# Optimization experiments

Hardware: AMD Instinct MI355X
Metric: run time of the kernel (lower is better)

The kernel has to match this reference:

```python
import jax, jax.numpy as jnp
import numpy as np

R = 45        # num_dep_rels
L = 384       # sent_len
D = 512       # word representation dim = in_size*2
E_REL = 15    # dep_rel_emb_size
IN4 = 1024    # in_size*4
HOPS = 3
THRESH = 1e-06


def setup_inputs() -> dict:
    key = jax.random.key(0)
    ks = jax.random.split(key, 10)
    energy = jax.random.uniform(ks[0], (1, R, L, L), dtype=jnp.float32)
    word_h = jax.random.normal(ks[1], (1, L, D), dtype=jnp.float32)
    e1 = jax.random.normal(ks[2], (D,), dtype=jnp.float32)
    e2 = jax.random.normal(ks[3], (D,), dtype=jnp.float32)
    # learned params
    rel_embs = jax.random.normal(ks[4], (R, E_REL), dtype=jnp.float32)
    Wc = jax.random.normal(ks[5], (2 * D + E_REL, D), dtype=jnp.float32) * 0.02
    bc = jnp.zeros((D,), dtype=jnp.float32)
    Wk = jax.random.normal(ks[6], (HOPS, IN4, IN4), dtype=jnp.float32) * 0.02
    bk = jnp.zeros((HOPS, IN4), dtype=jnp.float32)
    Wh = jax.random.normal(ks[7], (HOPS, IN4, IN4), dtype=jnp.float32) * 0.02
    bh = jnp.zeros((HOPS, IN4), dtype=jnp.float32)
    return {"energy": energy, "word_h": word_h, "e1": e1, "e2": e2,
            "sent_len": L, "rel_embs": rel_embs, "Wc": Wc, "bc": bc,
            "Wk": Wk, "bk": bk, "Wh": Wh, "bh": bh}


def reference(energy, word_h, e1, e2, sent_len, rel_embs, Wc, bc, Wk, bk, Wh, bh):
    Ls = sent_len
    E = energy[0, :, :Ls, :Ls]                 # [R, L, L]
    marg = E.sum(axis=0)                       # [L, L] marginal energy
    # threshold back-off (try t, t/10, t/100 until some arc survives)
    m0 = marg > THRESH
    m1 = marg > THRESH * 0.1
    m2 = marg > THRESH * 0.01
    mask = jnp.where(m0.any(), m0, jnp.where(m1.any(), m1, m2))  # [L, L]

    H = word_h[0, :Ls]                         # [L, D]
    w = marg.reshape(-1)                       # [L*L] arc weights
    # rel embedding per arc: sum_r E[r,h,d] * rel_embs[r,e]
    rels = jnp.einsum('rhd,re->hde', E, rel_embs).reshape(Ls * Ls, E_REL)
    head_t = jnp.repeat(H, Ls, axis=0) * w[:, None]   # [L*L, D]
    dep_t = jnp.tile(H, (Ls, 1)) * w[:, None]         # [L*L, D]
    arc_in = jnp.concatenate([head_t, rels, dep_t], axis=1)  # [L*L, 2D+15]
    mem_bank = jax.nn.leaky_relu(arc_in @ Wc + bc)    # [L*L, D] (dropout=eval)
    maskf = mask.reshape(-1)                          # [L*L]

    # multi-hop memory attention; filtered-out arcs get zero attention weight
    inputs = jnp.concatenate([e1, e2])                # [1024]
    for i in range(HOPS):
        kv = inputs @ Wk[i] + bk[i]                   # [1024]
        k_, v_ = jnp.split(kv, 2)                     # chunk along dim 0
        k_ = jnp.tanh(k_)
        v_ = jax.nn.leaky_relu(v_)
        scores = jnp.where(maskf, mem_bank @ k_, -1e30)  # [L*L]
        dist = jax.nn.softmax(scores)
        mem_rep = dist @ mem_bank                     # [D]
        inputs = jax.nn.leaky_relu(jnp.concatenate([v_, mem_rep]) @ Wh[i] + bh[i])
    return inputs
```

## Files before the change

### kernel.cpp

```cpp
#include <hip/hip_runtime.h>
#include <hip/hip_bf16.h>
#include <cstdint>
#include <cstddef>

#define LL      147456
#define NBLK    768
#define CHB     12
#define NPACK   288

typedef __attribute__((ext_vector_type(8))) short  short8;
typedef __attribute__((ext_vector_type(4))) float  f32x4;

#define EPACK_OFF   0u
#define MARG_OFF    14155776u
#define A_OFF       14745600u
#define BTC_OFF     15532032u
#define UTGP_OFF    16318464u
#define XIN_OFF     16367616u
#define KBUF_OFF    16371712u
#define VBUF_OFF    16373760u
#define PM_OFF      16377856u
#define PL_OFF      16380928u
#define PACC_OFF    16384000u
#define BLKF_OFF    17956864u

#define SKIP_LD     20.0f
#define PV_EPS      1e-8f

static __device__ __forceinline__ ushort f2bf(float x) {
  uint u = __float_as_uint(x);
  return (ushort)((u + 0x7fffu + ((u >> 16) & 1u)) >> 16);
}
static __device__ __forceinline__ float lrelu(float x) { return fmaxf(x, 0.01f * x); }

__global__ __launch_bounds__(256) void k_prep(
    const float* __restrict__ E, uint4* __restrict__ ep,
    float* __restrict__ marg, int* __restrict__ blkflags,
    const float* __restrict__ H, const float* __restrict__ Wc,
    const float* __restrict__ rel, const float* __restrict__ bc,
    float* __restrict__ A, float* __restrict__ Btc, uint4* __restrict__ Utgp) {
  __shared__ float Hs[4][512];
  __shared__ float Ps[4][512];
  __shared__ int fsh;
  int b = blockIdx.x, t = threadIdx.x;
  if (b < 192) {
    bool roleA = (b < 96);
    int g0 = (roleA ? b : b - 96) * 4;
    const float* Wcp = Wc + (size_t)(roleA ? 0 : 527) * 512;
    for (int i = t; i < 4 * 512; i += 256) Hs[i >> 9][i & 511] = H[(size_t)g0 * 512 + i];
    __syncthreads();
    int cq = t & 127, q = t >> 7;
    int c0 = cq * 4;
    f32x4 acc[4];
#pragma unroll
    for (int i = 0; i < 4; ++i) acc[i] = (f32x4){0.f, 0.f, 0.f, 0.f};
    for (int k = q * 256; k < q * 256 + 256; ++k) {
      f32x4 wv = *(const f32x4*)&Wcp[(size_t)k * 512 + c0];
#pragma unroll
      for (int i = 0; i < 4; ++i) { float hv = Hs[i][k]; acc[i] += hv * wv; }
    }
    if (q == 1) {
#pragma unroll
      for (int i = 0; i < 4; ++i) *(f32x4*)&Ps[i][c0] = acc[i];
    }
    __syncthreads();
    if (q == 0) {
#pragma unroll
      for (int i = 0; i < 4; ++i) {
        acc[i] += *(const f32x4*)&Ps[i][c0];
        if (roleA) {
          *(f32x4*)&A[(size_t)(g0 + i) * 512 + c0] = acc[i];
        } else {
#pragma unroll
          for (int j = 0; j < 4; ++j) Btc[(size_t)(c0 + j) * 384 + (g0 + i)] = acc[i][j];
        }
      }
    }
  } else if (b == 192) {
    for (int c = t; c < 512; c += 256) {
      float uv[48];
#pragma unroll
      for (int k = 0; k < 45; ++k) {
        float s = 0.f;
#pragma unroll
        for (int e = 0; e < 15; ++e) s += rel[k * 15 + e] * Wc[(size_t)(512 + e) * 512 + c];
        uv[k] = s;
      }
      uv[45] = bc[c]; uv[46] = 0.f; uv[47] = 0.f;
#pragma unroll
      for (int g = 0; g < 6; ++g) {
        uint w[4];
#pragma unroll
        for (int p = 0; p < 4; ++p)
          w[p] = (uint)f2bf(uv[g * 8 + 2 * p]) | ((uint)f2bf(uv[g * 8 + 2 * p + 1]) << 16);
        uint4 v; v.x = w[0]; v.y = w[1]; v.z = w[2]; v.w = w[3];
        Utgp[g * 512 + c] = v;
      }
    }
  } else {
    if (t == 0) fsh = 0;
    int bp = b - 193;
    size_t hd0 = (size_t)bp * 512 + 2 * t;
    float2 ev[46];
#pragma unroll
    for (int r = 0; r < 45; ++r) ev[r] = *(const float2*)&E[(size_t)r * LL + hd0];
    ev[45] = make_float2(1.0f, 1.0f);
    float s0 = 0.f, s1 = 0.f;
#pragma unroll
    for (int r = 0; r < 45; ++r) { s0 += ev[r].x; s1 += ev[r].y; }
#pragma unroll
    for (int o = 0; o < 6; ++o) {
      uint wa[4], wb[4];
#pragma unroll
      for (int p = 0; p < 4; ++p) {
        int r0 = 8 * o + 2 * p, r1 = r0 + 1;
        float a0 = (r0 < 46) ? ev[r0].x : 0.f, a1 = (r1 < 46) ? ev[r1].x : 0.f;
        float b0 = (r0 < 46) ? ev[r0].y : 0.f, b1 = (r1 < 46) ? ev[r1].y : 0.f;
        wa[p] = (uint)f2bf(a0) | ((uint)f2bf(a1) << 16);
        wb[p] = (uint)f2bf(b0) | ((uint)f2bf(b1) << 16);
      }
      uint4 va; va.x = wa[0]; va.y = wa[1]; va.z = wa[2]; va.w = wa[3];
      uint4 vb; vb.x = wb[0]; vb.y = wb[1]; vb.z = wb[2]; vb.w = wb[3];
      ep[(size_t)o * LL + hd0] = va;
      ep[(size_t)o * LL + hd0 + 1] = vb;
    }
    *(float2*)&marg[hd0] = make_float2(s0, s1);
    int f = (s0 > 1e-6f ? 1 : 0) | (s0 > 1e-7f ? 2 : 0) | (s0 > 1e-8f ? 4 : 0)
          | (s1 > 1e-6f ? 1 : 0) | (s1 > 1e-7f ? 2 : 0) | (s1 > 1e-8f ? 4 : 0);
#pragma unroll
    for (int d = 1; d < 64; d <<= 1) f |= __shfl_xor(f, d);
    __syncthreads();
    if ((t & 63) == 0) atomicOr(&fsh, f);
    __syncthreads();
    if (t == 0) blkflags[bp] = fsh;
  }
}

__global__ __launch_bounds__(256) void k_gemv(const float* __restrict__ W, const float* __restrict__ bias,
                                              const float* __restrict__ xA, const float* __restrict__ xB,
                                              float* __restrict__ kbuf, float* __restrict__ vbuf) {
  __shared__ float xs[1024];
  __shared__ float red[256];
  int t = threadIdx.x;
  for (int i = t; i < 1024; i += 256) xs[i] = (i < 512) ? xA[i] : xB[i - 512];
  __syncthreads();
  int jj = t & 15, kq = t >> 4;
  int j = blockIdx.x * 16 + jj;
  float acc = 0.f;
#pragma unroll 8
  for (int k = kq * 64; k < kq * 64 + 64; ++k) acc = fmaf(xs[k], W[(size_t)k * 1024 + j], acc);
  red[kq * 16 + jj] = acc;
  __syncthreads();
  if (kq == 0) {
    float s = bias[j];
#pragma unroll
    for (int q = 0; q < 16; ++q) s += red[q * 16 + jj];
    if (j < 512) kbuf[j] = tanhf(s);
    else vbuf[j - 512] = lrelu(s);
  }
}

__global__ __launch_bounds__(256, 3) void k_fused(
    const uint4* __restrict__ ep, const float* __restrict__ marg,
    const float* __restrict__ A, const float* __restrict__ Btc,
    const uint4* __restrict__ Utgp, const int* __restrict__ blkflags,
    const float* __restrict__ kvec,
    float* __restrict__ pm, float* __restrict__ pl, float* __restrict__ pacc) {
  __shared__ __align__(16) uint4 uthF[6 * 512];
  __shared__ float sbuf[CHB * 16];
  __shared__ float redw[8];
  __shared__ float paccs[256];
  __shared__ int fsh;
  int t = threadIdx.x, b = blockIdx.x;
  int dbt = b >> 5, hg = b & 31;
  int dbase = dbt * 16, h0 = hg * CHB;
  int lane = t & 63, wid = t >> 6;
  int l15 = lane & 15, qq = lane >> 4;

  if (t == 0) fsh = 0;
  for (int i = t; i < 6 * 512; i += 256) uthF[i] = Utgp[i];
  int f = 0;
  for (int i = t; i < NPACK; i += 256) f |= blkflags[i];
#pragma unroll
  for (int d = 1; d < 64; d <<= 1) f |= __shfl_xor(f, d);

  const short8 zero8 = (short8){0, 0, 0, 0, 0, 0, 0, 0};
  short8 a0[3], a1[3];
  f32x4 wq[3];
#pragma unroll
  for (int k3 = 0; k3 < 3; ++k3) {
    int h = h0 + wid * 3 + k3;
    int hda = h * 384 + dbase + l15;
    uint4 r0 = ep[(size_t)qq * LL + hda];
    a0[k3] = *(short8*)&r0;
    if (qq < 2) { uint4 r1 = ep[(size_t)(4 + qq) * LL + hda]; a1[k3] = *(short8*)&r1; }
    else a1[k3] = zero8;
    wq[k3] = *(const f32x4*)&marg[h * 384 + dbase + qq * 4];
  }
  __syncthreads();
  if ((t & 63) == 0) atomicOr(&fsh, f);

  float sp[3][4];
#pragma unroll
  for (int k3 = 0; k3 < 3; ++k3)
#pragma unroll
    for (int j = 0; j < 4; ++j) sp[k3][j] = 0.f;

  for (int half = 0; half < 2; ++half) {
    float kreg[16];
#pragma unroll
    for (int tt = 0; tt < 16; ++tt) kreg[tt] = kvec[half * 256 + tt * 16 + l15];
#pragma unroll 4
    for (int tt = 0; tt < 16; ++tt) {
      int c = half * 256 + tt * 16 + l15;
      short8 b0 = *(short8*)&uthF[qq * 512 + c];
      short8 b1 = (qq < 2) ? *(short8*)&uthF[(4 + qq) * 512 + c] : zero8;
      f32x4 btv = *(const f32x4*)&Btc[(size_t)c * 384 + dbase + qq * 4];
      const float* Ap = &A[(size_t)(h0 + wid * 3) * 512 + c];
      float av[3]; av[0] = Ap[0]; av[1] = Ap[512]; av[2] = Ap[1024];
#pragma unroll
      for (int k3 = 0; k3 < 3; ++k3) {
        f32x4 cc = (f32x4){0.f, 0.f, 0.f, 0.f};
        cc = __builtin_amdgcn_mfma_f32_16x16x32_bf16(a0[k3], b0, cc, 0, 0, 0);
        cc = __builtin_amdgcn_mfma_f32_16x16x32_bf16(a1[k3], b1, cc, 0, 0, 0);
        float aw = av[k3];
        float x0 = cc[0] + wq[k3][0] * (aw + btv[0]); float mb0 = fmaxf(x0, 0.01f * x0);
        float x1 = cc[1] + wq[k3][1] * (aw + btv[1]); float mb1 = fmaxf(x1, 0.01f * x1);
        float x2 = cc[2] + wq[k3][2] * (aw + btv[2]); float mb2 = fmaxf(x2, 0.01f * x2);
        float x3 = cc[3] + wq[k3][3] * (aw + btv[3]); float mb3 = fmaxf(x3, 0.01f * x3);
        sp[k3][0] = fmaf(mb0, kreg[tt], sp[k3][0]);
        sp[k3][1] = fmaf(mb1, kreg[tt], sp[k3][1]);
        sp[k3][2] = fmaf(mb2, kreg[tt], sp[k3][2]);
        sp[k3][3] = fmaf(mb3, kreg[tt], sp[k3][3]);
      }
    }
  }
#pragma unroll
  for (int k3 = 0; k3 < 3; ++k3)
#pragma unroll
    for (int j = 0; j < 4; ++j) {
#pragma unroll
      for (int d = 1; d < 16; d <<= 1) sp[k3][j] += __shfl_xor(sp[k3][j], d);
    }
  __syncthreads();
  float thr = (fsh & 1) ? 1e-6f : ((fsh & 2) ? 1e-7f : 1e-8f);
  if (l15 == 0) {
#pragma unroll
    for (int k3 = 0; k3 < 3; ++k3) {
      int base = (wid * 3 + k3) * 16 + qq * 4;
#pragma unroll
      for (int j = 0; j < 4; ++j)
        sbuf[base + j] = (wq[k3][j] > thr) ? sp[k3][j] : -1e30f;
    }
  }
  __syncthreads();

  float sv = (t < CHB * 16) ? sbuf[t] : -1e30f;
  float m = sv;
#pragma unroll
  for (int d = 1; d < 64; d <<= 1) m = fmaxf(m, __shfl_xor(m, d));
  if (lane == 0) redw[wid] = m;
  __syncthreads();
  float mloc = fmaxf(fmaxf(redw[0], redw[1]), fmaxf(redw[2], redw[3]));
  float e = (t < CHB * 16) ? __expf(sv - mloc) : 0.f;
#pragma unroll
  for (int d = 1; d < 64; d <<= 1) e += __shfl_xor(e, d);
  if (lane == 0) redw[4 + wid] = e;
  __syncthreads();
  if (t == 0) { pm[b] = mloc; pl[b] = redw[4] + redw[5] + redw[6] + redw[7]; }

  float pvw[3][4];
  float lmax = 0.f;
#pragma unroll
  for (int k3 = 0; k3 < 3; ++k3)
#pragma unroll
    for (int j = 0; j < 4; ++j) {
      float p = __expf(sbuf[(wid * 3 + k3) * 16 + qq * 4 + j] - mloc);
      pvw[k3][j] = p;
      lmax = fmaxf(lmax, p);
    }
  bool active = !__all(lmax < PV_EPS);

  for (int half = 0; half < 2; ++half) {
    paccs[t] = 0.f;
    __syncthreads();
    if (active) {
#pragma unroll 4
      for (int tt = 0; tt < 16; ++tt) {
        int c = half * 256 + tt * 16 + l15;
        short8 b0 = *(short8*)&uthF[qq * 512 + c];
        short8 b1 = (qq < 2) ? *(short8*)&uthF[(4 + qq) * 512 + c] : zero8;
        f32x4 btv = *(const f32x4*)&Btc[(size_t)c * 384 + dbase + qq * 4];
        const float* Ap = &A[(size_t)(h0 + wid * 3) * 512 + c];
        float av[3]; av[0] = Ap[0]; av[1] = Ap[512]; av[2] = Ap[1024];
        float acc_t = 0.f;
#pragma unroll
        for (int k3 = 0; k3 < 3; ++k3) {
          f32x4 cc = (f32x4){0.f, 0.f, 0.f, 0.f};
          cc = __builtin_amdgcn_mfma_f32_16x16x32_bf16(a0[k3], b0, cc, 0, 0, 0);
          cc = __builtin_amdgcn_mfma_f32_16x16x32_bf16(a1[k3], b1, cc, 0, 0, 0);
          float aw = av[k3];
          float x0 = cc[0] + wq[k3][0] * (aw + btv[0]); float mb0 = fmaxf(x0, 0.01f * x0);
          float x1 = cc[1] + wq[k3][1] * (aw + btv[1]); float mb1 = fmaxf(x1, 0.01f * x1);
          float x2 = cc[2] + wq[k3][2] * (aw + btv[2]); float mb2 = fmaxf(x2, 0.01f * x2);
          float x3 = cc[3] + wq[k3][3] * (aw + btv[3]); float mb3 = fmaxf(x3, 0.01f * x3);
          acc_t = fmaf(pvw[k3][0], mb0, fmaf(pvw[k3][1], mb1,
                  fmaf(pvw[k3][2], mb2, fmaf(pvw[k3][3], mb3, acc_t))));
        }
        acc_t += __shfl_xor(acc_t, 16);
        acc_t += __shfl_xor(acc_t, 32);
        if (lane < 16) atomicAdd(&paccs[tt * 16 + l15], acc_t);
      }
    }
    __syncthreads();
    pacc[(size_t)b * 512 + half * 256 + t] = paccs[t];
    __syncthreads();
  }
}

__global__ __launch_bounds__(256) void k_gemvc(
    const float* __restrict__ W, const float* __restrict__ bias,
    const float* __restrict__ vbuf, const float* __restrict__ pm,
    const float* __restrict__ pl, const float* __restrict__ pacc,
    float* __restrict__ outA, float* __restrict__ out2) {
  __shared__ float xs[1024];
  __shared__ float sc[NBLK];
  __shared__ int slist[NBLK];
  __shared__ int scnt_sh;
  __shared__ float redm[8];
  __shared__ float red[256];
  int t = threadIdx.x;
  int lane = t & 63, wid = t >> 6;

  float m = -1e30f;
  for (int i = t; i < NBLK; i += 256) m = fmaxf(m, pm[i]);
#pragma unroll
  for (int d = 1; d < 64; d <<= 1) m = fmaxf(m, __shfl_xor(m, d));
  if (lane == 0) redm[wid] = m;
  __syncthreads();
  float M = fmaxf(fmaxf(redm[0], redm[1]), fmaxf(redm[2], redm[3]));
  float ls = 0.f;
  for (int i = t; i < NBLK; i += 256) {
    float d = pm[i] - M;
    float e = (d < -SKIP_LD) ? 0.f : __expf(d);
    sc[i] = e;
    ls += e * pl[i];
  }
#pragma unroll
  for (int d = 1; d < 64; d <<= 1) ls += __shfl_xor(ls, d);
  if (lane == 0) redm[4 + wid] = ls;
  __syncthreads();
  float L = redm[4] + redm[5] + redm[6] + redm[7];

  if (wid == 0) {
    int cnt = 0;
#pragma unroll
    for (int rnd = 0; rnd < NBLK / 64; ++rnd) {
      int bb = rnd * 64 + lane;
      bool p = sc[bb] > 0.f;
      unsigned long long mask = __ballot(p);
      int off = __popcll(mask & ((1ull << lane) - 1ull));
      if (p) slist[cnt + off] = bb;
      cnt += __popcll(mask);
    }
    if (lane == 0) scnt_sh = cnt;
  }
  __syncthreads();
  int S = scnt_sh;
  for (int c = t; c < 512; c += 256) xs[c] = vbuf[c];
#pragma unroll
  for (int half = 0; half < 2; ++half) {
    int c = t + half * 256;
    float s = 0.f;
    for (int k = 0; k < S; ++k) {
      int bb = slist[k];
      s += pacc[(size_t)bb * 512 + c] * sc[bb];
    }
    xs[512 + c] = s / L;
  }
  __syncthreads();

  int jj = t & 15, kq = t >> 4;
  int j = blockIdx.x * 16 + jj;
  float acc = 0.f;
#pragma unroll 8
  for (int k = kq * 64; k < kq * 64 + 64; ++k) acc = fmaf(xs[k], W[(size_t)k * 1024 + j], acc);
  red[kq * 16 + jj] = acc;
  __syncthreads();
  if (kq == 0) {
    float s = bias[j];
#pragma unroll
    for (int q = 0; q < 16; ++q) s += red[q * 16 + jj];
    float rv = lrelu(s);
    outA[j] = rv;
    if (out2) out2[j] = rv;
  }
}

extern "C" void kernel_launch(void* const* d_in, const int* in_sizes, int n_in,
                              void* d_out, int out_size, void* d_ws, size_t ws_size,
                              hipStream_t stream) {
  const float* E   = (const float*)d_in[0];
  const float* H   = (const float*)d_in[1];
  const float* e1  = (const float*)d_in[2];
  const float* e2  = (const float*)d_in[3];
  const float* rel = (const float*)d_in[5];
  const float* Wc  = (const float*)d_in[6];
  const float* bc  = (const float*)d_in[7];
  const float* Wk  = (const float*)d_in[8];
  const float* bk  = (const float*)d_in[9];
  const float* Wh  = (const float*)d_in[10];
  const float* bh  = (const float*)d_in[11];

  char* ws = (char*)d_ws;
  uint4*  ep     = (uint4*)(ws + EPACK_OFF);
  float*  marg   = (float*)(ws + MARG_OFF);
  float*  Abuf   = (float*)(ws + A_OFF);
  float*  Btc    = (float*)(ws + BTC_OFF);
  uint4*  Utgp   = (uint4*)(ws + UTGP_OFF);
  float*  xin    = (float*)(ws + XIN_OFF);
  float*  kbuf   = (float*)(ws + KBUF_OFF);
  float*  vbuf   = (float*)(ws + VBUF_OFF);
  float*  pm     = (float*)(ws + PM_OFF);
  float*  pl     = (float*)(ws + PL_OFF);
  float*  pacc   = (float*)(ws + PACC_OFF);
  int*    blkf   = (int*)(ws + BLKF_OFF);

  k_prep<<<481, 256, 0, stream>>>(E, ep, marg, blkf, H, Wc, rel, bc, Abuf, Btc, Utgp);

  for (int hop = 0; hop < 3; ++hop) {
    const float* Wki = Wk + (size_t)hop * 1024 * 1024;
    const float* bki = bk + (size_t)hop * 1024;
    const float* Whi = Wh + (size_t)hop * 1024 * 1024;
    const float* bhi = bh + (size_t)hop * 1024;
    k_gemv<<<64, 256, 0, stream>>>(Wki, bki, hop == 0 ? e1 : xin,
                                   hop == 0 ? e2 : xin + 512, kbuf, vbuf);
    k_fused<<<NBLK, 256, 0, stream>>>(ep, marg, Abuf, Btc, Utgp, blkf, kbuf,
                                      pm, pl, pacc);
    k_gemvc<<<64, 256, 0, stream>>>(Whi, bhi, vbuf, pm, pl, pacc, xin,
                                    hop == 2 ? (float*)d_out : (float*)nullptr);
  }
}
```

Before: 191.2 us.

## Split fused score/PV kernel into two passes to skip low-weight blocks globally

The fused attention kernel is split into a scores kernel, which writes raw masked scores plus per-block max and sum, and a separate PV kernel. The PV kernel first computes the global max over all block maxima and exits early for blocks whose max is far below it. Previously a block could only skip based on its own local max. This adds a kernel launch per hop, a small global round trip for the scores, and reloads of the packed embedding and LDS data in the second kernel.

```diff
diff --git a/kernel.cpp b/kernel.cpp
--- a/kernel.cpp
+++ b/kernel.cpp
@@ -23,6 +23,7 @@
 #define PL_OFF      16380928u
 #define PACC_OFF    16384000u
 #define BLKF_OFF    17956864u
+#define SRAW_OFF    17958016u
 
 #define SKIP_LD     20.0f
 #define PV_EPS      1e-8f
@@ -160,16 +161,15 @@
   }
 }
 
-__global__ __launch_bounds__(256, 3) void k_fused(
+__global__ __launch_bounds__(256, 3) void k_scores(
     const uint4* __restrict__ ep, const float* __restrict__ marg,
     const float* __restrict__ A, const float* __restrict__ Btc,
     const uint4* __restrict__ Utgp, const int* __restrict__ blkflags,
     const float* __restrict__ kvec,
-    float* __restrict__ pm, float* __restrict__ pl, float* __restrict__ pacc) {
+    float* __restrict__ pm, float* __restrict__ pl, float* __restrict__ sraw) {
   __shared__ __align__(16) uint4 uthF[6 * 512];
   __shared__ float sbuf[CHB * 16];
   __shared__ float redw[8];
-  __shared__ float paccs[256];
   __shared__ int fsh;
   int t = threadIdx.x, b = blockIdx.x;
   int dbt = b >> 5, hg = b & 31;
@@ -266,8 +266,54 @@
 #pragma unroll
   for (int d = 1; d < 64; d <<= 1) e += __shfl_xor(e, d);
   if (lane == 0) redw[4 + wid] = e;
+  if (t < CHB * 16) sraw[(size_t)b * 192 + t] = sv;
   __syncthreads();
   if (t == 0) { pm[b] = mloc; pl[b] = redw[4] + redw[5] + redw[6] + redw[7]; }
+}
+
+__global__ __launch_bounds__(256, 3) void k_pv(
+    const uint4* __restrict__ ep, const float* __restrict__ marg,
+    const float* __restrict__ A, const float* __restrict__ Btc,
+    const uint4* __restrict__ Utgp, const float* __restrict__ pm,
+    const float* __restrict__ sraw, float* __restrict__ pacc) {
+  __shared__ __align__(16) uint4 uthF[6 * 512];
+  __shared__ float pbuf[CHB * 16];
+  __shared__ float paccs[256];
+  __shared__ float redm[4];
+  int t = threadIdx.x, b = blockIdx.x;
+  int lane = t & 63, wid = t >> 6;
+
+  float m = -1e30f;
+  for (int i = t; i < NBLK; i += 256) m = fmaxf(m, pm[i]);
+#pragma unroll
+  for (int d = 1; d < 64; d <<= 1) m = fmaxf(m, __shfl_xor(m, d));
+  if (lane == 0) redm[wid] = m;
+  __syncthreads();
+  float M = fmaxf(fmaxf(redm[0], redm[1]), fmaxf(redm[2], redm[3]));
+  float pmb = pm[b];
+  if (pmb - M < -SKIP_LD) return;
+
+  int dbt = b >> 5, hg = b & 31;
+  int dbase = dbt * 16, h0 = hg * CHB;
+  int l15 = lane & 15, qq = lane >> 4;
+
+  for (int i = t; i < 6 * 512; i += 256) uthF[i] = Utgp[i];
+  if (t < CHB * 16) pbuf[t] = __expf(sraw[(size_t)b * 192 + t] - pmb);
+
+  const short8 zero8 = (short8){0, 0, 0, 0, 0, 0, 0, 0};
+  short8 a0[3], a1[3];
+  f32x4 wq[3];
+#pragma unroll
+  for (int k3 = 0; k3 < 3; ++k3) {
+    int h = h0 + wid * 3 + k3;
+    int hda = h * 384 + dbase + l15;
+    uint4 r0 = ep[(size_t)qq * LL + hda];
+    a0[k3] = *(short8*)&r0;
+    if (qq < 2) { uint4 r1 = ep[(size_t)(4 + qq) * LL + hda]; a1[k3] = *(short8*)&r1; }
+    else a1[k3] = zero8;
+    wq[k3] = *(const f32x4*)&marg[h * 384 + dbase + qq * 4];
+  }
+  __syncthreads();
 
   float pvw[3][4];
   float lmax = 0.f;
@@ -275,7 +321,7 @@
   for (int k3 = 0; k3 < 3; ++k3)
 #pragma unroll
     for (int j = 0; j < 4; ++j) {
-      float p = __expf(sbuf[(wid * 3 + k3) * 16 + qq * 4 + j] - mloc);
+      float p = pbuf[(wid * 3 + k3) * 16 + qq * 4 + j];
       pvw[k3][j] = p;
       lmax = fmaxf(lmax, p);
     }
@@ -425,6 +471,7 @@
   float*  pl     = (float*)(ws + PL_OFF);
   float*  pacc   = (float*)(ws + PACC_OFF);
   int*    blkf   = (int*)(ws + BLKF_OFF);
+  float*  sraw   = (float*)(ws + SRAW_OFF);
 
   k_prep<<<481, 256, 0, stream>>>(E, ep, marg, blkf, H, Wc, rel, bc, Abuf, Btc, Utgp);
 
@@ -435,8 +482,9 @@
     const float* bhi = bh + (size_t)hop * 1024;
     k_gemv<<<64, 256, 0, stream>>>(Wki, bki, hop == 0 ? e1 : xin,
                                    hop == 0 ? e2 : xin + 512, kbuf, vbuf);
-    k_fused<<<NBLK, 256, 0, stream>>>(ep, marg, Abuf, Btc, Utgp, blkf, kbuf,
-                                      pm, pl, pacc);
+    k_scores<<<NBLK, 256, 0, stream>>>(ep, marg, Abuf, Btc, Utgp, blkf, kbuf,
+                                       pm, pl, sraw);
+    k_pv<<<NBLK, 256, 0, stream>>>(ep, marg, Abuf, Btc, Utgp, pm, sraw, pacc);
     k_gemvc<<<64, 256, 0, stream>>>(Whi, bhi, vbuf, pm, pl, pacc, xin,
                                     hop == 2 ? (float*)d_out : (float*)nullptr);
   }
```

Measured after the change: 194.1 us. About the same (+1.5%).
